# Optimization experiments

Hardware: AMD Instinct MI355X
Metric: run time of the kernel (lower is better)

The kernel has to match this reference:

```python
import jax, jax.numpy as jnp
import numpy as np


def setup_inputs() -> dict:
    key = jax.random.key(0)
    k1, k2, k3, k4 = jax.random.split(key, 4)
    B, S, D_IN, D_OUT = 4, 2048, 4096, 16384
    x = jax.random.normal(k1, (B, S, D_IN), dtype=jnp.float32)
    # compressed (int8-style) weight, stored [in_features, out_features] per Conv1D convention
    w_q = jax.random.randint(k2, (D_IN, D_OUT), -127, 127, dtype=jnp.int32)
    # per-output-channel dequant scale
    scale = jax.random.uniform(k3, (D_OUT,), dtype=jnp.float32) * 0.01 + 1e-4
    bias = jax.random.normal(k4, (D_OUT,), dtype=jnp.float32)
    return {"x": x, "w_q": w_q, "scale": scale, "bias": bias}


def reference(x, w_q, scale, bias):
    # Dequantize compressed weight: W[i, o] = w_q[i, o] * scale[o]
    w = w_q.astype(jnp.float32) * scale[None, :]  # [D_in, D_out]
    # Conv1D forward: y = x @ W + b
    y = jnp.einsum('bsi,io->bso', x, w) + bias
    return y
```

## Files before the change

kernel.cpp:

```cpp
#include <hip/hip_runtime.h>


#define M_DIM 8192
#define K_DIM 4096
#define N_DIM 16384

#define BM 256
#define BN 256
#define BK 64
#define NT (K_DIM / BK)
#define NWG ((M_DIM / BM) * (N_DIM / BN))

typedef unsigned short u16;
typedef __attribute__((ext_vector_type(8))) short short8;
typedef __attribute__((ext_vector_type(4))) float floatx4;

__device__ __forceinline__ u16 f2bf(float f) {
    unsigned int u = __builtin_bit_cast(unsigned int, f);
    u += 0x7fffu + ((u >> 16) & 1u);
    return (u16)(u >> 16);
}

__global__ __launch_bounds__(256) void cvt_x_kernel(const float4* __restrict__ x,
                                                    uint4* __restrict__ out) {
    int i = blockIdx.x * 256 + threadIdx.x;
    float4 a = x[2 * i];
    float4 b = x[2 * i + 1];
    uint4 o;
    o.x = (unsigned)f2bf(a.x) | ((unsigned)f2bf(a.y) << 16);
    o.y = (unsigned)f2bf(a.z) | ((unsigned)f2bf(a.w) << 16);
    o.z = (unsigned)f2bf(b.x) | ((unsigned)f2bf(b.y) << 16);
    o.w = (unsigned)f2bf(b.z) | ((unsigned)f2bf(b.w) << 16);
    out[i] = o;
}

__global__ __launch_bounds__(256) void transpose_wq(const int* __restrict__ wq,
                                                    u16* __restrict__ wT) {
    __shared__ u16 tile[64][65];
    const int n0 = blockIdx.x * 64;
    const int k0 = blockIdx.y * 64;
    const int tx = threadIdx.x;
    const int ty = threadIdx.y;
    #pragma unroll
    for (int r = 0; r < 4; ++r) {
        int kl = ty + 16 * r;
        const int4 v = *(const int4*)(wq + (size_t)(k0 + kl) * N_DIM + n0 + tx * 4);
        tile[kl][tx * 4 + 0] = f2bf((float)v.x);
        tile[kl][tx * 4 + 1] = f2bf((float)v.y);
        tile[kl][tx * 4 + 2] = f2bf((float)v.z);
        tile[kl][tx * 4 + 3] = f2bf((float)v.w);
    }
    __syncthreads();
    #pragma unroll
    for (int r = 0; r < 4; ++r) {
        int nl = ty + 16 * r;
        ushort4 o;
        o.x = tile[tx * 4 + 0][nl];
        o.y = tile[tx * 4 + 1][nl];
        o.z = tile[tx * 4 + 2][nl];
        o.w = tile[tx * 4 + 3][nl];
        *(ushort4*)(wT + (size_t)(n0 + nl) * K_DIM + k0 + tx * 4) = o;
    }
}

__device__ __forceinline__ void async_copy16(const u16* gptr, u16* ldsptr) {
    __builtin_amdgcn_global_load_lds(
        (const __attribute__((address_space(1))) void*)gptr,
        (__attribute__((address_space(3))) void*)ldsptr,
        16, 0, 0);
}

__global__ __launch_bounds__(512, 2) void gemm_bf16(const u16* __restrict__ A,
                                                    const u16* __restrict__ Bt,
                                                    const float* __restrict__ scale,
                                                    const float* __restrict__ bias,
                                                    float* __restrict__ C) {
    __shared__ u16 smem[65536];

    const int tid  = threadIdx.x;
    const int lane = tid & 63;
    const int wave = tid >> 6;
    const int wr   = wave >> 2;
    const int wc   = wave & 3;
    const int fr   = lane & 15;
    const int quad = lane >> 4;

    int wg = blockIdx.x;
    wg = (wg & 7) * (NWG / 8) + (wg >> 3);
    const int grp = wg >> 9;
    const int rem = wg & 511;
    const int by  = grp * 8 + (rem & 7);
    const int bx  = rem >> 3;
    const int m0 = by * BM;
    const int n0 = bx * BN;

    const int sw   = fr & 7;
    const int sl0  = (quad ^ sw) * 8;
    const int sl1  = sl0 ^ 32;
    const int rA   = fr * 64;
    const int aBase0 = wr * 8192;
    const int bBase0 = 16384 + (wc >> 1) * 8192 + (wc & 1) * 4096;

    const int srow  = tid >> 3;
    const int sslot = ((tid & 7) ^ (srow & 7)) * 8;
    const int ldst  = tid * 8;

#define STAGE_A(t_, h_, p_) do {                                               \
    const u16* g_ = A + (size_t)(m0 + (h_) * 128 + srow) * K_DIM + (t_) * BK + sslot; \
    u16* l_ = smem + (p_) * 32768 + (h_) * 8192 + ldst;                        \
    async_copy16(g_, l_);                                                      \
    async_copy16(g_ + (size_t)64 * K_DIM, l_ + 4096);                          \
} while (0)

#define STAGE_B(t_, h_, p_) do {                                               \
    const u16* g_ = Bt + (size_t)(n0 + (h_) * 128 + srow) * K_DIM + (t_) * BK + sslot; \
    u16* l_ = smem + (p_) * 32768 + 16384 + (h_) * 8192 + ldst;                \
    async_copy16(g_, l_);                                                      \
    async_copy16(g_ + (size_t)64 * K_DIM, l_ + 4096);                          \
} while (0)

    floatx4 acc[8][4];
    #pragma unroll
    for (int i = 0; i < 8; ++i)
        #pragma unroll
        for (int j = 0; j < 4; ++j)
            acc[i][j] = (floatx4){0.f, 0.f, 0.f, 0.f};

    STAGE_A(0, 0, 0); STAGE_A(0, 1, 0); STAGE_B(0, 0, 0); STAGE_B(0, 1, 0);
    STAGE_B(1, 0, 1); STAGE_B(1, 1, 1);
    asm volatile("s_waitcnt vmcnt(4)" ::: "memory");
    __builtin_amdgcn_s_barrier();
    __builtin_amdgcn_sched_barrier(0);

    short8 af[4], bfv[4];

    for (int t = 0; t < NT; ++t) {
        const int p  = t & 1;
        const int pn = p ^ 1;
        const u16* SA = smem + p * 32768 + aBase0;
        const u16* SB = smem + p * 32768 + bBase0;

        #pragma unroll
        for (int i = 0; i < 4; ++i)
            af[i] = *(const short8*)(SA + i * 1024 + rA + sl0);
        #pragma unroll
        for (int j = 0; j < 4; ++j)
            bfv[j] = *(const short8*)(SB + j * 1024 + rA + sl0);
        if (t + 1 < NT) { STAGE_A(t + 1, 0, pn); STAGE_A(t + 1, 1, pn); }
        __builtin_amdgcn_s_barrier();
        asm volatile("s_waitcnt lgkmcnt(0)" ::: "memory");
        __builtin_amdgcn_s_setprio(1);
        #pragma unroll
        for (int i = 0; i < 4; ++i)
            #pragma unroll
            for (int j = 0; j < 4; ++j)
                acc[i][j] = __builtin_amdgcn_mfma_f32_16x16x32_bf16(af[i], bfv[j], acc[i][j], 0, 0, 0);
        __builtin_amdgcn_s_setprio(0);
        __builtin_amdgcn_s_barrier();
        __builtin_amdgcn_sched_barrier(0);

        #pragma unroll
        for (int i = 0; i < 4; ++i)
            af[i] = *(const short8*)(SA + (i + 4) * 1024 + rA + sl0);
        __builtin_amdgcn_s_barrier();
        asm volatile("s_waitcnt lgkmcnt(0)" ::: "memory");
        __builtin_amdgcn_s_setprio(1);
        #pragma unroll
        for (int i = 0; i < 4; ++i)
            #pragma unroll
            for (int j = 0; j < 4; ++j)
                acc[i + 4][j] = __builtin_amdgcn_mfma_f32_16x16x32_bf16(af[i], bfv[j], acc[i + 4][j], 0, 0, 0);
        __builtin_amdgcn_s_setprio(0);
        __builtin_amdgcn_s_barrier();
        __builtin_amdgcn_sched_barrier(0);

        #pragma unroll
        for (int i = 0; i < 4; ++i)
            af[i] = *(const short8*)(SA + i * 1024 + rA + sl1);
        #pragma unroll
        for (int j = 0; j < 4; ++j)
            bfv[j] = *(const short8*)(SB + j * 1024 + rA + sl1);
        __builtin_amdgcn_s_barrier();
        asm volatile("s_waitcnt lgkmcnt(0)" ::: "memory");
        __builtin_amdgcn_s_setprio(1);
        #pragma unroll
        for (int i = 0; i < 4; ++i)
            #pragma unroll
            for (int j = 0; j < 4; ++j)
                acc[i][j] = __builtin_amdgcn_mfma_f32_16x16x32_bf16(af[i], bfv[j], acc[i][j], 0, 0, 0);
        __builtin_amdgcn_s_setprio(0);
        __builtin_amdgcn_s_barrier();
        __builtin_amdgcn_sched_barrier(0);

        #pragma unroll
        for (int i = 0; i < 4; ++i)
            af[i] = *(const short8*)(SA + (i + 4) * 1024 + rA + sl1);
        if (t + 2 < NT) { STAGE_B(t + 2, 0, p); STAGE_B(t + 2, 1, p); }
        __builtin_amdgcn_s_barrier();
        asm volatile("s_waitcnt lgkmcnt(0)" ::: "memory");
        __builtin_amdgcn_s_setprio(1);
        #pragma unroll
        for (int i = 0; i < 4; ++i)
            #pragma unroll
            for (int j = 0; j < 4; ++j)
                acc[i + 4][j] = __builtin_amdgcn_mfma_f32_16x16x32_bf16(af[i], bfv[j], acc[i + 4][j], 0, 0, 0);
        __builtin_amdgcn_s_setprio(0);
        if (t < NT - 2) {
            asm volatile("s_waitcnt vmcnt(4)" ::: "memory");
        } else if (t == NT - 2) {
            asm volatile("s_waitcnt vmcnt(0)" ::: "memory");
        }
        __builtin_amdgcn_s_barrier();
        __builtin_amdgcn_sched_barrier(0);
    }

    #pragma unroll
    for (int j = 0; j < 4; ++j) {
        const int col = n0 + wc * 64 + j * 16 + fr;
        const float s = scale[col];
        const float b = bias[col];
        #pragma unroll
        for (int i = 0; i < 8; ++i) {
            const int rowb = m0 + wr * 128 + i * 16 + quad * 4;
            #pragma unroll
            for (int r = 0; r < 4; ++r)
                C[(size_t)(rowb + r) * N_DIM + col] = acc[i][j][r] * s + b;
        }
    }
#undef STAGE_A
#undef STAGE_B
}

extern "C" void kernel_launch(void* const* d_in, const int* in_sizes, int n_in,
                              void* d_out, int out_size, void* d_ws, size_t ws_size,
                              hipStream_t stream) {
    const float* x     = (const float*)d_in[0];
    const int*   wq    = (const int*)d_in[1];
    const float* scale = (const float*)d_in[2];
    const float* bias  = (const float*)d_in[3];
    float* y = (float*)d_out;

    u16* wT = (u16*)d_ws;
    u16* xb = (u16*)((char*)d_ws + (size_t)N_DIM * K_DIM * 2);

    cvt_x_kernel<<<(M_DIM * (size_t)K_DIM) / (256 * 8), 256, 0, stream>>>(
        (const float4*)x, (uint4*)xb);
    transpose_wq<<<dim3(N_DIM / 64, K_DIM / 64), dim3(16, 16), 0, stream>>>(wq, wT);
    gemm_bf16<<<dim3(NWG), 512, 0, stream>>>(xb, wT, scale, bias, y);
}
```

Measured before the change: 1.715 ms.

## Drop per-phase barriers in GEMM main loop and use incremental global pointers

```diff
diff --git a/kernel.cpp b/kernel.cpp
--- a/kernel.cpp
+++ b/kernel.cpp
@@ -105,19 +105,8 @@
     const int sslot = ((tid & 7) ^ (srow & 7)) * 8;
     const int ldst  = tid * 8;
 
-#define STAGE_A(t_, h_, p_) do {                                               \
-    const u16* g_ = A + (size_t)(m0 + (h_) * 128 + srow) * K_DIM + (t_) * BK + sslot; \
-    u16* l_ = smem + (p_) * 32768 + (h_) * 8192 + ldst;                        \
-    async_copy16(g_, l_);                                                      \
-    async_copy16(g_ + (size_t)64 * K_DIM, l_ + 4096);                          \
-} while (0)
-
-#define STAGE_B(t_, h_, p_) do {                                               \
-    const u16* g_ = Bt + (size_t)(n0 + (h_) * 128 + srow) * K_DIM + (t_) * BK + sslot; \
-    u16* l_ = smem + (p_) * 32768 + 16384 + (h_) * 8192 + ldst;                \
-    async_copy16(g_, l_);                                                      \
-    async_copy16(g_ + (size_t)64 * K_DIM, l_ + 4096);                          \
-} while (0)
+    const u16* gA = A  + (size_t)(m0 + srow) * K_DIM + sslot + BK;
+    const u16* gB = Bt + (size_t)(n0 + srow) * K_DIM + sslot + 2 * BK;
 
     floatx4 acc[8][4];
     #pragma unroll
@@ -126,90 +115,110 @@
         for (int j = 0; j < 4; ++j)
             acc[i][j] = (floatx4){0.f, 0.f, 0.f, 0.f};
 
-    STAGE_A(0, 0, 0); STAGE_A(0, 1, 0); STAGE_B(0, 0, 0); STAGE_B(0, 1, 0);
-    STAGE_B(1, 0, 1); STAGE_B(1, 1, 1);
+    {
+        const u16* a0 = A  + (size_t)(m0 + srow) * K_DIM + sslot;
+        const u16* b0 = Bt + (size_t)(n0 + srow) * K_DIM + sslot;
+        #pragma unroll
+        for (int r = 0; r < 4; ++r)
+            async_copy16(a0 + (size_t)(64 * r) * K_DIM, smem + ldst + r * 4096);
+        #pragma unroll
+        for (int r = 0; r < 4; ++r)
+            async_copy16(b0 + (size_t)(64 * r) * K_DIM, smem + 16384 + ldst + r * 4096);
+        #pragma unroll
+        for (int r = 0; r < 4; ++r)
+            async_copy16(b0 + BK + (size_t)(64 * r) * K_DIM,
+                         smem + 32768 + 16384 + ldst + r * 4096);
+    }
     asm volatile("s_waitcnt vmcnt(4)" ::: "memory");
+    __builtin_amdgcn_sched_barrier(0);
     __builtin_amdgcn_s_barrier();
     __builtin_amdgcn_sched_barrier(0);
 
-    short8 af[4], bfv[4];
-
     for (int t = 0; t < NT; ++t) {
-        const int p  = t & 1;
-        const int pn = p ^ 1;
-        const u16* SA = smem + p * 32768 + aBase0;
-        const u16* SB = smem + p * 32768 + bBase0;
-
-        #pragma unroll
-        for (int i = 0; i < 4; ++i)
-            af[i] = *(const short8*)(SA + i * 1024 + rA + sl0);
+        const int p     = t & 1;
+        const int pOff  = p << 15;
+        const int pnOff = pOff ^ 32768;
+        const u16* SA = smem + pOff + aBase0;
+        const u16* SB = smem + pOff + bBase0;
+
+        if (t + 1 < NT) {
+            u16* d = smem + pnOff + ldst;
+            #pragma unroll
+            for (int r = 0; r < 4; ++r)
+                async_copy16(gA + (size_t)(64 * r) * K_DIM, d + r * 4096);
+        }
+        gA += BK;
+
+        short8 a0[4], a1[4], b0[4], b1[4];
+        #pragma unroll
+        for (int i = 0; i < 4; ++i)
+            a0[i] = *(const short8*)(SA + i * 1024 + rA + sl0);
         #pragma unroll
         for (int j = 0; j < 4; ++j)
-            bfv[j] = *(const short8*)(SB + j * 1024 + rA + sl0);
-        if (t + 1 < NT) { STAGE_A(t + 1, 0, pn); STAGE_A(t + 1, 1, pn); }
+            b0[j] = *(const short8*)(SB + j * 1024 + rA + sl0);
+        __builtin_amdgcn_s_setprio(1);
+        #pragma unroll
+        for (int i = 0; i < 4; ++i)
+            #pragma unroll
+            for (int j = 0; j < 4; ++j)
+                acc[i][j] = __builtin_amdgcn_mfma_f32_16x16x32_bf16(a0[i], b0[j], acc[i][j], 0, 0, 0);
+        __builtin_amdgcn_s_setprio(0);
+
+        #pragma unroll
+        for (int i = 0; i < 4; ++i)
+            a1[i] = *(const short8*)(SA + (i + 4) * 1024 + rA + sl0);
+        __builtin_amdgcn_s_setprio(1);
+        #pragma unroll
+        for (int i = 0; i < 4; ++i)
+            #pragma unroll
+            for (int j = 0; j < 4; ++j)
+                acc[i + 4][j] = __builtin_amdgcn_mfma_f32_16x16x32_bf16(a1[i], b0[j], acc[i + 4][j], 0, 0, 0);
+        __builtin_amdgcn_s_setprio(0);
+
+        #pragma unroll
+        for (int i = 0; i < 4; ++i)
+            a0[i] = *(const short8*)(SA + i * 1024 + rA + sl1);
+        #pragma unroll
+        for (int j = 0; j < 4; ++j)
+            b1[j] = *(const short8*)(SB + j * 1024 + rA + sl1);
+        __builtin_amdgcn_s_setprio(1);
+        #pragma unroll
+        for (int i = 0; i < 4; ++i)
+            #pragma unroll
+            for (int j = 0; j < 4; ++j)
+                acc[i][j] = __builtin_amdgcn_mfma_f32_16x16x32_bf16(a0[i], b1[j], acc[i][j], 0, 0, 0);
+        __builtin_amdgcn_s_setprio(0);
+
+        #pragma unroll
+        for (int i = 0; i < 4; ++i)
+            a1[i] = *(const short8*)(SA + (i + 4) * 1024 + rA + sl1);
+
+        __builtin_amdgcn_sched_barrier(0);
         __builtin_amdgcn_s_barrier();
-        asm volatile("s_waitcnt lgkmcnt(0)" ::: "memory");
-        __builtin_amdgcn_s_setprio(1);
-        #pragma unroll
-        for (int i = 0; i < 4; ++i)
-            #pragma unroll
-            for (int j = 0; j < 4; ++j)
-                acc[i][j] = __builtin_amdgcn_mfma_f32_16x16x32_bf16(af[i], bfv[j], acc[i][j], 0, 0, 0);
-        __builtin_amdgcn_s_setprio(0);
-        __builtin_amdgcn_s_barrier();
-        __builtin_amdgcn_sched_barrier(0);
-
-        #pragma unroll
-        for (int i = 0; i < 4; ++i)
-            af[i] = *(const short8*)(SA + (i + 4) * 1024 + rA + sl0);
-        __builtin_amdgcn_s_barrier();
-        asm volatile("s_waitcnt lgkmcnt(0)" ::: "memory");
-        __builtin_amdgcn_s_setprio(1);
-        #pragma unroll
-        for (int i = 0; i < 4; ++i)
-            #pragma unroll
-            for (int j = 0; j < 4; ++j)
-                acc[i + 4][j] = __builtin_amdgcn_mfma_f32_16x16x32_bf16(af[i], bfv[j], acc[i + 4][j], 0, 0, 0);
-        __builtin_amdgcn_s_setprio(0);
-        __builtin_amdgcn_s_barrier();
-        __builtin_amdgcn_sched_barrier(0);
-
-        #pragma unroll
-        for (int i = 0; i < 4; ++i)
-            af[i] = *(const short8*)(SA + i * 1024 + rA + sl1);
-        #pragma unroll
-        for (int j = 0; j < 4; ++j)
-            bfv[j] = *(const short8*)(SB + j * 1024 + rA + sl1);
-        __builtin_amdgcn_s_barrier();
-        asm volatile("s_waitcnt lgkmcnt(0)" ::: "memory");
-        __builtin_amdgcn_s_setprio(1);
-        #pragma unroll
-        for (int i = 0; i < 4; ++i)
-            #pragma unroll
-            for (int j = 0; j < 4; ++j)
-                acc[i][j] = __builtin_amdgcn_mfma_f32_16x16x32_bf16(af[i], bfv[j], acc[i][j], 0, 0, 0);
-        __builtin_amdgcn_s_setprio(0);
-        __builtin_amdgcn_s_barrier();
-        __builtin_amdgcn_sched_barrier(0);
-
-        #pragma unroll
-        for (int i = 0; i < 4; ++i)
-            af[i] = *(const short8*)(SA + (i + 4) * 1024 + rA + sl1);
-        if (t + 2 < NT) { STAGE_B(t + 2, 0, p); STAGE_B(t + 2, 1, p); }
-        __builtin_amdgcn_s_barrier();
-        asm volatile("s_waitcnt lgkmcnt(0)" ::: "memory");
-        __builtin_amdgcn_s_setprio(1);
-        #pragma unroll
-        for (int i = 0; i < 4; ++i)
-            #pragma unroll
-            for (int j = 0; j < 4; ++j)
-                acc[i + 4][j] = __builtin_amdgcn_mfma_f32_16x16x32_bf16(af[i], bfv[j], acc[i + 4][j], 0, 0, 0);
-        __builtin_amdgcn_s_setprio(0);
+        __builtin_amdgcn_sched_barrier(0);
+
+        if (t + 2 < NT) {
+            u16* d = smem + pOff + 16384 + ldst;
+            #pragma unroll
+            for (int r = 0; r < 4; ++r)
+                async_copy16(gB + (size_t)(64 * r) * K_DIM, d + r * 4096);
+        }
+        gB += BK;
+
+        __builtin_amdgcn_s_setprio(1);
+        #pragma unroll
+        for (int i = 0; i < 4; ++i)
+            #pragma unroll
+            for (int j = 0; j < 4; ++j)
+                acc[i + 4][j] = __builtin_amdgcn_mfma_f32_16x16x32_bf16(a1[i], b1[j], acc[i + 4][j], 0, 0, 0);
+        __builtin_amdgcn_s_setprio(0);
+
         if (t < NT - 2) {
             asm volatile("s_waitcnt vmcnt(4)" ::: "memory");
         } else if (t == NT - 2) {
             asm volatile("s_waitcnt vmcnt(0)" ::: "memory");
         }
+        __builtin_amdgcn_sched_barrier(0);
         __builtin_amdgcn_s_barrier();
         __builtin_amdgcn_sched_barrier(0);
     }
@@ -227,8 +236,6 @@
                 C[(size_t)(rowb + r) * N_DIM + col] = acc[i][j][r] * s + b;
         }
     }
-#undef STAGE_A
-#undef STAGE_B
 }
 
 extern "C" void kernel_launch(void* const* d_in, const int* in_sizes, int n_in,
```

Result: faster. 1.667 ms (-2.8%).
